# Kernel optimization log

Hardware: AMD Instinct MI355X
Metric: run time of the kernel (lower is better)

## Reference

```python
import jax, jax.numpy as jnp
import numpy as np

HEADS, HEAD_DIM = 8, 32
FOLD_W = FOLD_H = 8
PW = PH = 2  # proposal_w/h -> M = PW*PH centers per region


def setup_inputs() -> dict:
    key = jax.random.key(0)
    ks = jax.random.split(key, 8)
    dim, hd = 96, HEADS * HEAD_DIM
    return {
        "x": jax.random.normal(ks[0], (16, dim, 64, 64), jnp.float32),
        "Wf": jax.random.normal(ks[1], (hd, dim), jnp.float32) * 0.05,
        "bf": jax.random.normal(ks[2], (hd,), jnp.float32) * 0.01,
        "Wv": jax.random.normal(ks[3], (hd, dim), jnp.float32) * 0.05,
        "bv": jax.random.normal(ks[4], (hd,), jnp.float32) * 0.01,
        "Wp": jax.random.normal(ks[5], (dim, hd), jnp.float32) * 0.05,
        "bp": jax.random.normal(ks[6], (dim,), jnp.float32) * 0.01,
        "sim_alpha": jnp.ones((1,), jnp.float32),
        "sim_beta": jnp.zeros((1,), jnp.float32),
    }


def _l2norm(t):
    # matches torch F.normalize(dim=-1, eps=1e-12)
    n = jnp.maximum(jnp.linalg.norm(t, axis=-1, keepdims=True), 1e-12)
    return t / n


def _cluster_forward(x, Wf, bf, Wv, bv, Wp, bp, sim_alpha, sim_beta):
    B, C, W, H = x.shape
    # 1x1 convs
    v = jnp.einsum("bchw,oc->bohw", x, Wv) + bv[None, :, None, None]
    f = jnp.einsum("bchw,oc->bohw", x, Wf) + bf[None, :, None, None]

    def split_heads(t):  # b (e c) w h -> (b e) c w h
        b = t.shape[0]
        return t.reshape(b, HEADS, HEAD_DIM, W, H).reshape(b * HEADS, HEAD_DIM, W, H)

    f, v = split_heads(f), split_heads(v)

    def fold(t):  # b c (f1 w) (f2 h) -> (b f1 f2) c w h
        b, c, w0, h0 = t.shape
        ws, hs = w0 // FOLD_W, h0 // FOLD_H
        t = t.reshape(b, c, FOLD_W, ws, FOLD_H, hs)
        return t.transpose(0, 2, 4, 1, 3, 5).reshape(b * FOLD_W * FOLD_H, c, ws, hs)

    f, v = fold(f), fold(v)
    b, c, w, h = f.shape

    def pool(t):  # AdaptiveMaxPool2d((PW,PH)); divides evenly -> block max
        return t.reshape(b, c, PW, w // PW, PH, h // PH).max(axis=(3, 5))

    centers = pool(f).reshape(b, c, PW * PH).transpose(0, 2, 1)       # [b,M,c]
    value_centers = pool(v).reshape(b, c, PW * PH).transpose(0, 2, 1)  # [b,M,c]
    pts = f.reshape(b, c, w * h).transpose(0, 2, 1)                    # [b,N,c]

    cos = jnp.einsum("bmc,bnc->bmn", _l2norm(centers), _l2norm(pts))
    sim = jax.nn.sigmoid(sim_beta + sim_alpha * cos)                   # [b,M,N]

    # hard assignment: each point keeps only its best center
    idx = jnp.argmax(sim, axis=1)                                      # [b,N]
    mask = jax.nn.one_hot(idx, sim.shape[1], dtype=sim.dtype)          # [b,N,M]
    mask = jnp.transpose(mask, (0, 2, 1))                              # [b,M,N]
    sim = sim * mask

    value2 = v.reshape(b, c, w * h).transpose(0, 2, 1)                 # [b,N,c]
    # gather points -> centers
    agg = (jnp.einsum("bnc,bmn->bmc", value2, sim) + value_centers) / (
        mask.sum(axis=-1, keepdims=True) + 1.0
    )
    # dispatch centers -> points
    out = jnp.einsum("bmc,bmn->bnc", agg, sim)                         # [b,N,c]
    out = out.transpose(0, 2, 1).reshape(b, c, w, h)

    # unfold regions back
    bb = b // (FOLD_W * FOLD_H)
    out = out.reshape(bb, FOLD_W, FOLD_H, c, w, h).transpose(0, 3, 1, 4, 2, 5)
    out = out.reshape(bb, c, FOLD_W * w, FOLD_H * h)
    # merge heads: (b e) c w h -> b (e c) w h
    out = out.reshape(bb // HEADS, HEADS * HEAD_DIM, W, H)
    out = jnp.einsum("bchw,oc->bohw", out, Wp) + bp[None, :, None, None]
    return out


def reference(x, Wf, bf, Wv, bv, Wp, bp, sim_alpha, sim_beta):
    return _cluster_forward(x, Wf, bf, Wv, bv, Wp, bp, sim_alpha, sim_beta)
```

## Files before the change

### kernel.cpp

```cpp
#include <hip/hip_runtime.h>
#include <math.h>


#define TPB 256

__global__ __launch_bounds__(TPB, 4)
void cc_main(const float* __restrict__ x,
             const float* __restrict__ Wf, const float* __restrict__ bf,
             const float* __restrict__ Wv, const float* __restrict__ bv,
             const float* __restrict__ Wp,
             const float* __restrict__ salpha, const float* __restrict__ sbeta,
             float* __restrict__ cd)
{
    __shared__ __align__(16) float smem[8320];
    __shared__ float cfs[2][132], cvs[2][132], swb[2][256], aggs[2][132];
    __shared__ float2 bib[2][64];
    __shared__ float cnts[2][4];

    const int t    = threadIdx.x;
    const int lane = t & 63;
    const int wid  = __builtin_amdgcn_readfirstlane(t >> 6);
    const int tc   = t >> 4;
    const int tp   = t & 15;
    const int blk  = blockIdx.x;
    const int f1   = blk & 7;
    const int f2   = (blk >> 3) & 7;
    const int heg  = (blk >> 6) & 3;
    const int bb   = blk >> 8;
    const int fold = f1*8 + f2;

    const float* xb = x + (size_t)bb*96*4096 + (size_t)(f1*8)*64 + f2*8;

    float acc[8][4];
    {
        const float* bsrc = (tc < 8) ? (bf + heg*64 + tc*8)
                                     : (bv + heg*64 + (tc-8)*8);
        float4 b0 = *(const float4*)bsrc;
        float4 b1 = *(const float4*)(bsrc + 4);
        #pragma unroll
        for (int i = 0; i < 4; ++i) {
            acc[0][i]=b0.x; acc[1][i]=b0.y; acc[2][i]=b0.z; acc[3][i]=b0.w;
            acc[4][i]=b1.x; acc[5][i]=b1.y; acc[6][i]=b1.z; acc[7][i]=b1.w;
        }
    }

    int xoff[2], xdst[2];
    #pragma unroll
    for (int i = 0; i < 2; ++i) {
        int fl = i*256 + t;
        int kl = fl >> 4, sg = fl & 15;
        xoff[i] = kl*4096 + (sg >> 1)*64 + (sg & 1)*4;
        xdst[i] = 4096 + kl*64 + sg*4;
    }
    int wdst[4];
    const float* wptr[4];
    #pragma unroll
    for (int i = 0; i < 4; ++i) {
        int fl = i*256 + t;
        int rr = fl & 127, kq = fl >> 7;
        wptr[i] = ((rr < 64) ? (Wf + (size_t)(heg*64 + rr)*96)
                             : (Wv + (size_t)(heg*64 + rr - 64)*96)) + kq*4;
        wdst[i] = (kq*4)*128 + rr;
    }

    float4 pxr[2], pwr[4];
    #pragma unroll
    for (int i = 0; i < 2; ++i) pxr[i] = *(const float4*)(xb + xoff[i]);
    #pragma unroll
    for (int i = 0; i < 4; ++i) pwr[i] = *(const float4*)(wptr[i]);
    #pragma unroll
    for (int i = 0; i < 2; ++i) *(float4*)&smem[xdst[i]] = pxr[i];
    #pragma unroll
    for (int i = 0; i < 4; ++i) {
        smem[wdst[i]      ] = pwr[i].x;
        smem[wdst[i] + 128] = pwr[i].y;
        smem[wdst[i] + 256] = pwr[i].z;
        smem[wdst[i] + 384] = pwr[i].w;
    }
    __syncthreads();

    for (int kc = 0; ; ) {
        if (kc < 64) {
            #pragma unroll
            for (int i = 0; i < 2; ++i)
                pxr[i] = *(const float4*)(xb + (kc+32)*4096 + xoff[i]);
            #pragma unroll
            for (int i = 0; i < 4; ++i)
                pwr[i] = *(const float4*)(wptr[i] + kc + 32);
        }
        #pragma unroll 4
        for (int k = 0; k < 32; ++k) {
            float4 wa  = *(const float4*)&smem[k*128 + tc*8];
            float4 wb4 = *(const float4*)&smem[k*128 + tc*8 + 4];
            float4 xq  = *(const float4*)&smem[4096 + k*64 + tp*4];
            float xv[4] = {xq.x, xq.y, xq.z, xq.w};
            #pragma unroll
            for (int i = 0; i < 4; ++i) {
                acc[0][i] = fmaf(wa.x,  xv[i], acc[0][i]);
                acc[1][i] = fmaf(wa.y,  xv[i], acc[1][i]);
                acc[2][i] = fmaf(wa.z,  xv[i], acc[2][i]);
                acc[3][i] = fmaf(wa.w,  xv[i], acc[3][i]);
                acc[4][i] = fmaf(wb4.x, xv[i], acc[4][i]);
                acc[5][i] = fmaf(wb4.y, xv[i], acc[5][i]);
                acc[6][i] = fmaf(wb4.z, xv[i], acc[6][i]);
                acc[7][i] = fmaf(wb4.w, xv[i], acc[7][i]);
            }
        }
        if (kc == 64) break;
        __syncthreads();
        #pragma unroll
        for (int i = 0; i < 2; ++i) *(float4*)&smem[xdst[i]] = pxr[i];
        #pragma unroll
        for (int i = 0; i < 4; ++i) {
            smem[wdst[i]      ] = pwr[i].x;
            smem[wdst[i] + 128] = pwr[i].y;
            smem[wdst[i] + 256] = pwr[i].z;
            smem[wdst[i] + 384] = pwr[i].w;
        }
        __syncthreads();
        kc += 32;
    }

    const float alpha = salpha[0], beta = sbeta[0];
    __syncthreads();
    #pragma unroll
    for (int j = 0; j < 8; ++j)
        #pragma unroll
        for (int i2 = 0; i2 < 4; ++i2)
            smem[(tc*8 + j)*65 + tp*4 + i2] = acc[j][i2];
    __syncthreads();

    if (wid < 2) {
        const int he = wid, slot = he;
        {
            int m = lane >> 4, c0 = (lane & 15)*2;
            int pw = m >> 1, ph = m & 1;
            #pragma unroll
            for (int cc = 0; cc < 2; ++cc) {
                int c = c0 + cc;
                float mf = -3.402823466e38f, mv = -3.402823466e38f;
                #pragma unroll
                for (int a = 0; a < 4; ++a)
                    #pragma unroll
                    for (int b2 = 0; b2 < 4; ++b2) {
                        int n = (pw*4 + a)*8 + ph*4 + b2;
                        mf = fmaxf(mf, smem[(he*32 + c)*65 + n]);
                        mv = fmaxf(mv, smem[(64 + he*32 + c)*65 + n]);
                    }
                cfs[slot][m*33 + c] = mf;
                cvs[slot][m*33 + c] = mv;
            }
        }
        float d0=0,d1=0,d2=0,d3=0,pn=0,cn0=0,cn1=0,cn2=0,cn3=0;
        #pragma unroll 8
        for (int c = 0; c < 32; ++c) {
            float fv = smem[(he*32 + c)*65 + lane];
            float m0 = cfs[slot][c], m1 = cfs[slot][33+c];
            float m2 = cfs[slot][66+c], m3 = cfs[slot][99+c];
            d0 = fmaf(m0, fv, d0); d1 = fmaf(m1, fv, d1);
            d2 = fmaf(m2, fv, d2); d3 = fmaf(m3, fv, d3);
            pn = fmaf(fv, fv, pn);
            cn0 = fmaf(m0, m0, cn0); cn1 = fmaf(m1, m1, cn1);
            cn2 = fmaf(m2, m2, cn2); cn3 = fmaf(m3, m3, cn3);
        }
        float ip = 1.f / fmaxf(sqrtf(pn), 1e-12f);
        float z0 = beta + alpha*(d0*(1.f/fmaxf(sqrtf(cn0),1e-12f))*ip);
        float z1 = beta + alpha*(d1*(1.f/fmaxf(sqrtf(cn1),1e-12f))*ip);
        float z2 = beta + alpha*(d2*(1.f/fmaxf(sqrtf(cn2),1e-12f))*ip);
        float z3 = beta + alpha*(d3*(1.f/fmaxf(sqrtf(cn3),1e-12f))*ip);
        float s0 = 1.f/(1.f + expf(-z0));
        float s1 = 1.f/(1.f + expf(-z1));
        float s2 = 1.f/(1.f + expf(-z2));
        float s3 = 1.f/(1.f + expf(-z3));
        int bi = 0; float bvv = s0;
        if (s1 > bvv) { bvv = s1; bi = 1; }
        if (s2 > bvv) { bvv = s2; bi = 2; }
        if (s3 > bvv) { bvv = s3; bi = 3; }
        int cnt0 = __popcll(__ballot(bi == 0));
        int cnt1 = __popcll(__ballot(bi == 1));
        int cnt2 = __popcll(__ballot(bi == 2));
        int cnt3 = __popcll(__ballot(bi == 3));
        swb[slot][lane]       = (bi==0) ? bvv : 0.f;
        swb[slot][64 + lane]  = (bi==1) ? bvv : 0.f;
        swb[slot][128 + lane] = (bi==2) ? bvv : 0.f;
        swb[slot][192 + lane] = (bi==3) ? bvv : 0.f;
        bib[slot][lane] = make_float2(bvv, (float)bi);
        if (lane == 0) {
            cnts[slot][0] = (float)cnt0; cnts[slot][1] = (float)cnt1;
            cnts[slot][2] = (float)cnt2; cnts[slot][3] = (float)cnt3;
        }
    }
    __syncthreads();

    float* tb = cd + ((size_t)(bb*64 + fold))*4096;

    if (wid >= 2) {
        const int he = wid - 2, slot = he;
        const int cI = lane & 31;
        #pragma unroll
        for (int it = 0; it < 2; ++it) {
            int mm = it*2 + (lane >> 5);
            float s = 0.f;
            #pragma unroll 8
            for (int n2 = 0; n2 < 64; ++n2)
                s = fmaf(smem[(64 + he*32 + cI)*65 + n2],
                         swb[slot][mm*64 + n2], s);
            aggs[slot][mm*33 + cI] = (s + cvs[slot][mm*33 + cI])
                                   / (cnts[slot][mm] + 1.f);
        }
        float2 b2 = bib[slot][lane];
        *(float2*)&tb[3072 + (heg*2 + he)*128 + lane*2] = b2;
    }
    __syncthreads();

    #pragma unroll
    for (int it = 0; it < 3; ++it) {
        int idx = it*256 + t;
        int he  = (idx >= 384) ? 1 : 0;
        int rem = idx - he*384;
        int oc  = rem >> 2, m = rem & 3;
        const float* wp = Wp + (size_t)oc*256 + heg*64 + he*32;
        const float* ag = aggs[he] + m*33;
        float s = 0.f;
        #pragma unroll
        for (int c = 0; c < 32; ++c)
            s = fmaf(wp[c], ag[c], s);
        tb[(heg*2 + he)*384 + oc*4 + m] = s;
    }
}

__global__ __launch_bounds__(TPB, 8)
void cc_comb(const float* __restrict__ cd, const float* __restrict__ bp,
             float* __restrict__ out)
{
    __shared__ __align__(16) float ld[4096];
    const int t    = threadIdx.x;
    const int lane = t & 63;
    const int wid  = __builtin_amdgcn_readfirstlane(t >> 6);
    const int blk  = blockIdx.x;
    const int f1   = blk & 7;
    const int f2   = (blk >> 3) & 7;
    const int bb   = blk >> 6;
    const float* tb = cd + ((size_t)(bb*64 + f1*8 + f2))*4096;

    #pragma unroll
    for (int i = 0; i < 4; ++i) {
        float4 v = *(const float4*)(tb + (t*4 + i)*4);
        *(float4*)&ld[(t*4 + i)*4] = v;
    }
    __syncthreads();

    const int oc0 = wid*24;
    float acc[24];
    #pragma unroll
    for (int j = 0; j < 24; j += 4) {
        float4 b = *(const float4*)(bp + oc0 + j);
        acc[j]=b.x; acc[j+1]=b.y; acc[j+2]=b.z; acc[j+3]=b.w;
    }

    #pragma unroll
    for (int he = 0; he < 8; ++he) {
        float2 sv = *(const float2*)&ld[3072 + he*128 + lane*2];
        const int bi = (int)sv.y;
        const float s0 = (bi==0) ? sv.x : 0.f;
        const float s1 = (bi==1) ? sv.x : 0.f;
        const float s2 = (bi==2) ? sv.x : 0.f;
        const float s3 = (bi==3) ? sv.x : 0.f;
        const float* pr = &ld[he*384 + oc0*4];
        #pragma unroll
        for (int j = 0; j < 24; ++j) {
            float4 p = *(const float4*)(pr + j*4);
            acc[j] = fmaf(p.x, s0, acc[j]);
            acc[j] = fmaf(p.y, s1, acc[j]);
            acc[j] = fmaf(p.z, s2, acc[j]);
            acc[j] = fmaf(p.w, s3, acc[j]);
        }
    }

    const int r = lane >> 3, hh = lane & 7;
    const size_t ob = (size_t)bb*96*4096 + (size_t)(f1*8 + r)*64 + f2*8 + hh;
    #pragma unroll
    for (int j = 0; j < 24; ++j)
        out[ob + (size_t)(oc0 + j)*4096] = acc[j];
}

extern "C" void kernel_launch(void* const* d_in, const int* in_sizes, int n_in,
                              void* d_out, int out_size, void* d_ws, size_t ws_size,
                              hipStream_t stream) {
    (void)in_sizes; (void)n_in; (void)out_size; (void)ws_size;
    float* cd = (float*)d_ws;
    cc_main<<<dim3(4096), dim3(TPB), 0, stream>>>(
        (const float*)d_in[0],
        (const float*)d_in[1],
        (const float*)d_in[2],
        (const float*)d_in[3],
        (const float*)d_in[4],
        (const float*)d_in[5],
        (const float*)d_in[7],
        (const float*)d_in[8],
        cd);
    cc_comb<<<dim3(1024), dim3(TPB), 0, stream>>>(
        cd,
        (const float*)d_in[6],
        (float*)d_out);
}
```

Measured before the change: 211.5 us.

## Fuse combine stage into main kernel via atomic accumulation into bias-initialized output

Removes the separate combine kernel and workspace round-trip. A small init kernel fills the output with the projection bias, and each main block computes its two heads' contribution to every output channel and atomically adds it into the output. This avoids writing and re-reading the intermediate per-fold buffer. In exchange it issues four atomic adds per output element (one per head group), adds a barrier in the main kernel, and makes the float summation order nondeterministic.

```diff
diff --git a/kernel.cpp b/kernel.cpp
--- a/kernel.cpp
+++ b/kernel.cpp
@@ -3,6 +3,18 @@
 
 
 #define TPB 256
+
+__global__ __launch_bounds__(TPB, 8)
+void cc_init(const float* __restrict__ bp, float* __restrict__ out)
+{
+    const int oc = blockIdx.x % 96;
+    const float b = bp[oc];
+    const float4 v = make_float4(b, b, b, b);
+    float* o = out + (size_t)blockIdx.x * 4096 + threadIdx.x * 4;
+    #pragma unroll
+    for (int i = 0; i < 4; ++i)
+        *(float4*)(o + i*1024) = v;
+}
 
 __global__ __launch_bounds__(TPB, 4)
 void cc_main(const float* __restrict__ x,
@@ -10,7 +22,7 @@
              const float* __restrict__ Wv, const float* __restrict__ bv,
              const float* __restrict__ Wp,
              const float* __restrict__ salpha, const float* __restrict__ sbeta,
-             float* __restrict__ cd)
+             float* __restrict__ out)
 {
     __shared__ __align__(16) float smem[8320];
     __shared__ float cfs[2][132], cvs[2][132], swb[2][256], aggs[2][132];
@@ -27,7 +39,6 @@
     const int f2   = (blk >> 3) & 7;
     const int heg  = (blk >> 6) & 3;
     const int bb   = blk >> 8;
-    const int fold = f1*8 + f2;
 
     const float* xb = x + (size_t)bb*96*4096 + (size_t)(f1*8)*64 + f2*8;
 
@@ -192,8 +203,6 @@
     }
     __syncthreads();
 
-    float* tb = cd + ((size_t)(bb*64 + fold))*4096;
-
     if (wid >= 2) {
         const int he = wid - 2, slot = he;
         const int cI = lane & 31;
@@ -208,8 +217,6 @@
             aggs[slot][mm*33 + cI] = (s + cvs[slot][mm*33 + cI])
                                    / (cnts[slot][mm] + 1.f);
         }
-        float2 b2 = bib[slot][lane];
-        *(float2*)&tb[3072 + (heg*2 + he)*128 + lane*2] = b2;
     }
     __syncthreads();
 
@@ -225,70 +232,49 @@
         #pragma unroll
         for (int c = 0; c < 32; ++c)
             s = fmaf(wp[c], ag[c], s);
-        tb[(heg*2 + he)*384 + oc*4 + m] = s;
-    }
-}
-
-__global__ __launch_bounds__(TPB, 8)
-void cc_comb(const float* __restrict__ cd, const float* __restrict__ bp,
-             float* __restrict__ out)
-{
-    __shared__ __align__(16) float ld[4096];
-    const int t    = threadIdx.x;
-    const int lane = t & 63;
-    const int wid  = __builtin_amdgcn_readfirstlane(t >> 6);
-    const int blk  = blockIdx.x;
-    const int f1   = blk & 7;
-    const int f2   = (blk >> 3) & 7;
-    const int bb   = blk >> 6;
-    const float* tb = cd + ((size_t)(bb*64 + f1*8 + f2))*4096;
-
-    #pragma unroll
-    for (int i = 0; i < 4; ++i) {
-        float4 v = *(const float4*)(tb + (t*4 + i)*4);
-        *(float4*)&ld[(t*4 + i)*4] = v;
-    }
-    __syncthreads();
-
-    const int oc0 = wid*24;
-    float acc[24];
-    #pragma unroll
-    for (int j = 0; j < 24; j += 4) {
-        float4 b = *(const float4*)(bp + oc0 + j);
-        acc[j]=b.x; acc[j+1]=b.y; acc[j+2]=b.z; acc[j+3]=b.w;
-    }
-
-    #pragma unroll
-    for (int he = 0; he < 8; ++he) {
-        float2 sv = *(const float2*)&ld[3072 + he*128 + lane*2];
-        const int bi = (int)sv.y;
-        const float s0 = (bi==0) ? sv.x : 0.f;
-        const float s1 = (bi==1) ? sv.x : 0.f;
-        const float s2 = (bi==2) ? sv.x : 0.f;
-        const float s3 = (bi==3) ? sv.x : 0.f;
-        const float* pr = &ld[he*384 + oc0*4];
-        #pragma unroll
-        for (int j = 0; j < 24; ++j) {
-            float4 p = *(const float4*)(pr + j*4);
-            acc[j] = fmaf(p.x, s0, acc[j]);
-            acc[j] = fmaf(p.y, s1, acc[j]);
-            acc[j] = fmaf(p.z, s2, acc[j]);
-            acc[j] = fmaf(p.w, s3, acc[j]);
-        }
-    }
-
-    const int r = lane >> 3, hh = lane & 7;
-    const size_t ob = (size_t)bb*96*4096 + (size_t)(f1*8 + r)*64 + f2*8 + hh;
-    #pragma unroll
-    for (int j = 0; j < 24; ++j)
-        out[ob + (size_t)(oc0 + j)*4096] = acc[j];
+        smem[he*384 + oc*4 + m] = s;
+    }
+    __syncthreads();
+
+    {
+        const int oc0 = wid*24;
+        float con[24];
+        #pragma unroll
+        for (int j = 0; j < 24; ++j) con[j] = 0.f;
+        #pragma unroll
+        for (int he = 0; he < 2; ++he) {
+            float2 sv = bib[he][lane];
+            const int bi = (int)sv.y;
+            const float s0 = (bi==0) ? sv.x : 0.f;
+            const float s1 = (bi==1) ? sv.x : 0.f;
+            const float s2 = (bi==2) ? sv.x : 0.f;
+            const float s3 = (bi==3) ? sv.x : 0.f;
+            const float* pr = &smem[he*384 + oc0*4];
+            #pragma unroll
+            for (int j = 0; j < 24; ++j) {
+                float4 p = *(const float4*)(pr + j*4);
+                con[j] = fmaf(p.x, s0, con[j]);
+                con[j] = fmaf(p.y, s1, con[j]);
+                con[j] = fmaf(p.z, s2, con[j]);
+                con[j] = fmaf(p.w, s3, con[j]);
+            }
+        }
+        const int r = lane >> 3, hh = lane & 7;
+        const size_t ob = (size_t)bb*96*4096
+                        + (size_t)(f1*8 + r)*64 + f2*8 + hh;
+        #pragma unroll
+        for (int j = 0; j < 24; ++j)
+            atomicAdd(&out[ob + (size_t)(oc0 + j)*4096], con[j]);
+    }
 }
 
 extern "C" void kernel_launch(void* const* d_in, const int* in_sizes, int n_in,
                               void* d_out, int out_size, void* d_ws, size_t ws_size,
                               hipStream_t stream) {
-    (void)in_sizes; (void)n_in; (void)out_size; (void)ws_size;
-    float* cd = (float*)d_ws;
+    (void)in_sizes; (void)n_in; (void)out_size; (void)d_ws; (void)ws_size;
+    cc_init<<<dim3(1536), dim3(TPB), 0, stream>>>(
+        (const float*)d_in[6],
+        (float*)d_out);
     cc_main<<<dim3(4096), dim3(TPB), 0, stream>>>(
         (const float*)d_in[0],
         (const float*)d_in[1],
@@ -298,9 +284,5 @@
         (const float*)d_in[5],
         (const float*)d_in[7],
         (const float*)d_in[8],
-        cd);
-    cc_comb<<<dim3(1024), dim3(TPB), 0, stream>>>(
-        cd,
-        (const float*)d_in[6],
         (float*)d_out);
 }
```

New measurement: 264.7 us. 1.25x slower.

## Process two fold regions per block with 8x8 register tiles in projection GEMM

Applied to the files above, without the earlier changes.

Each block now covers two adjacent fold regions (128 pixels) instead of one, so the 1x1-conv GEMM uses an 8x8 per-thread register tile, doubling arithmetic per shared-memory load and halving weight reloads per pixel. The K chunk shrinks from 32 to 16 to keep shared memory within budget. The clustering epilogue then runs twice in a loop, once per fold. The grid is halved, and the larger accumulator tile raises register pressure, which may reduce occupancy under launch_bounds(256,4).

```diff
diff --git a/kernel.cpp b/kernel.cpp
--- a/kernel.cpp
+++ b/kernel.cpp
@@ -20,42 +20,38 @@
     const int t    = threadIdx.x;
     const int lane = t & 63;
     const int wid  = __builtin_amdgcn_readfirstlane(t >> 6);
-    const int tc   = t >> 4;
-    const int tp   = t & 15;
+    const int cg   = t >> 4;
+    const int pg   = t & 15;
     const int blk  = blockIdx.x;
     const int f1   = blk & 7;
-    const int f2   = (blk >> 3) & 7;
-    const int heg  = (blk >> 6) & 3;
-    const int bb   = blk >> 8;
-    const int fold = f1*8 + f2;
-
-    const float* xb = x + (size_t)bb*96*4096 + (size_t)(f1*8)*64 + f2*8;
-
-    float acc[8][4];
+    const int f2p  = (blk >> 3) & 3;
+    const int heg  = (blk >> 5) & 3;
+    const int bb   = blk >> 7;
+
+    const float* xb = x + (size_t)bb*96*4096 + (size_t)(f1*8)*64 + f2p*16;
+
+    float acc[8][8];
     {
-        const float* bsrc = (tc < 8) ? (bf + heg*64 + tc*8)
-                                     : (bv + heg*64 + (tc-8)*8);
-        float4 b0 = *(const float4*)bsrc;
-        float4 b1 = *(const float4*)(bsrc + 4);
-        #pragma unroll
-        for (int i = 0; i < 4; ++i) {
-            acc[0][i]=b0.x; acc[1][i]=b0.y; acc[2][i]=b0.z; acc[3][i]=b0.w;
-            acc[4][i]=b1.x; acc[5][i]=b1.y; acc[6][i]=b1.z; acc[7][i]=b1.w;
-        }
+        const float* bsrc = ((cg < 8) ? bf : bv) + heg*64 + (cg & 7)*8;
+        float4 b0 = *(const float4*)bsrc, b1 = *(const float4*)(bsrc + 4);
+        float bj[8] = {b0.x,b0.y,b0.z,b0.w,b1.x,b1.y,b1.z,b1.w};
+        #pragma unroll
+        for (int j = 0; j < 8; ++j)
+            #pragma unroll
+            for (int i = 0; i < 8; ++i) acc[j][i] = bj[j];
     }
 
     int xoff[2], xdst[2];
     #pragma unroll
     for (int i = 0; i < 2; ++i) {
         int fl = i*256 + t;
-        int kl = fl >> 4, sg = fl & 15;
-        xoff[i] = kl*4096 + (sg >> 1)*64 + (sg & 1)*4;
-        xdst[i] = 4096 + kl*64 + sg*4;
-    }
-    int wdst[4];
-    const float* wptr[4];
-    #pragma unroll
-    for (int i = 0; i < 4; ++i) {
+        int kl = fl >> 5, p4 = (fl & 31)*4;
+        xoff[i] = kl*4096 + ((p4 & 63) >> 3)*64 + (p4 >> 6)*8 + (p4 & 7);
+        xdst[i] = 2048 + kl*128 + p4;
+    }
+    int wdst[2]; const float* wptr[2];
+    #pragma unroll
+    for (int i = 0; i < 2; ++i) {
         int fl = i*256 + t;
         int rr = fl & 127, kq = fl >> 7;
         wptr[i] = ((rr < 64) ? (Wf + (size_t)(heg*64 + rr)*96)
@@ -63,15 +59,15 @@
         wdst[i] = (kq*4)*128 + rr;
     }
 
-    float4 pxr[2], pwr[4];
+    float4 pxr[2], pwr[2];
     #pragma unroll
     for (int i = 0; i < 2; ++i) pxr[i] = *(const float4*)(xb + xoff[i]);
     #pragma unroll
-    for (int i = 0; i < 4; ++i) pwr[i] = *(const float4*)(wptr[i]);
+    for (int i = 0; i < 2; ++i) pwr[i] = *(const float4*)(wptr[i]);
     #pragma unroll
     for (int i = 0; i < 2; ++i) *(float4*)&smem[xdst[i]] = pxr[i];
     #pragma unroll
-    for (int i = 0; i < 4; ++i) {
+    for (int i = 0; i < 2; ++i) {
         smem[wdst[i]      ] = pwr[i].x;
         smem[wdst[i] + 128] = pwr[i].y;
         smem[wdst[i] + 256] = pwr[i].z;
@@ -80,152 +76,155 @@
     __syncthreads();
 
     for (int kc = 0; ; ) {
-        if (kc < 64) {
+        if (kc < 80) {
             #pragma unroll
             for (int i = 0; i < 2; ++i)
-                pxr[i] = *(const float4*)(xb + (kc+32)*4096 + xoff[i]);
-            #pragma unroll
-            for (int i = 0; i < 4; ++i)
-                pwr[i] = *(const float4*)(wptr[i] + kc + 32);
+                pxr[i] = *(const float4*)(xb + (kc+16)*4096 + xoff[i]);
+            #pragma unroll
+            for (int i = 0; i < 2; ++i)
+                pwr[i] = *(const float4*)(wptr[i] + kc + 16);
         }
         #pragma unroll 4
-        for (int k = 0; k < 32; ++k) {
-            float4 wa  = *(const float4*)&smem[k*128 + tc*8];
-            float4 wb4 = *(const float4*)&smem[k*128 + tc*8 + 4];
-            float4 xq  = *(const float4*)&smem[4096 + k*64 + tp*4];
-            float xv[4] = {xq.x, xq.y, xq.z, xq.w};
-            #pragma unroll
-            for (int i = 0; i < 4; ++i) {
-                acc[0][i] = fmaf(wa.x,  xv[i], acc[0][i]);
-                acc[1][i] = fmaf(wa.y,  xv[i], acc[1][i]);
-                acc[2][i] = fmaf(wa.z,  xv[i], acc[2][i]);
-                acc[3][i] = fmaf(wa.w,  xv[i], acc[3][i]);
-                acc[4][i] = fmaf(wb4.x, xv[i], acc[4][i]);
-                acc[5][i] = fmaf(wb4.y, xv[i], acc[5][i]);
-                acc[6][i] = fmaf(wb4.z, xv[i], acc[6][i]);
-                acc[7][i] = fmaf(wb4.w, xv[i], acc[7][i]);
-            }
-        }
-        if (kc == 64) break;
+        for (int k = 0; k < 16; ++k) {
+            float4 wa = *(const float4*)&smem[k*128 + cg*8];
+            float4 wb = *(const float4*)&smem[k*128 + cg*8 + 4];
+            float4 xa = *(const float4*)&smem[2048 + k*128 + pg*8];
+            float4 xc = *(const float4*)&smem[2048 + k*128 + pg*8 + 4];
+            float wv[8] = {wa.x,wa.y,wa.z,wa.w,wb.x,wb.y,wb.z,wb.w};
+            float xv[8] = {xa.x,xa.y,xa.z,xa.w,xc.x,xc.y,xc.z,xc.w};
+            #pragma unroll
+            for (int j = 0; j < 8; ++j)
+                #pragma unroll
+                for (int i = 0; i < 8; ++i)
+                    acc[j][i] = fmaf(wv[j], xv[i], acc[j][i]);
+        }
+        if (kc == 80) break;
         __syncthreads();
         #pragma unroll
         for (int i = 0; i < 2; ++i) *(float4*)&smem[xdst[i]] = pxr[i];
         #pragma unroll
-        for (int i = 0; i < 4; ++i) {
+        for (int i = 0; i < 2; ++i) {
             smem[wdst[i]      ] = pwr[i].x;
             smem[wdst[i] + 128] = pwr[i].y;
             smem[wdst[i] + 256] = pwr[i].z;
             smem[wdst[i] + 384] = pwr[i].w;
         }
         __syncthreads();
-        kc += 32;
+        kc += 16;
     }
 
     const float alpha = salpha[0], beta = sbeta[0];
-    __syncthreads();
-    #pragma unroll
-    for (int j = 0; j < 8; ++j)
-        #pragma unroll
-        for (int i2 = 0; i2 < 4; ++i2)
-            smem[(tc*8 + j)*65 + tp*4 + i2] = acc[j][i2];
-    __syncthreads();
-
-    if (wid < 2) {
-        const int he = wid, slot = he;
-        {
-            int m = lane >> 4, c0 = (lane & 15)*2;
-            int pw = m >> 1, ph = m & 1;
-            #pragma unroll
-            for (int cc = 0; cc < 2; ++cc) {
-                int c = c0 + cc;
-                float mf = -3.402823466e38f, mv = -3.402823466e38f;
+
+    for (int fl = 0; fl < 2; ++fl) {
+        __syncthreads();
+        if ((pg >> 3) == fl) {
+            const int nb = (pg & 7)*8;
+            #pragma unroll
+            for (int j = 0; j < 8; ++j)
                 #pragma unroll
-                for (int a = 0; a < 4; ++a)
+                for (int i = 0; i < 8; ++i)
+                    smem[(cg*8 + j)*65 + nb + i] = acc[j][i];
+        }
+        __syncthreads();
+
+        if (wid < 2) {
+            const int he = wid, slot = he;
+            {
+                int m = lane >> 4, c0 = (lane & 15)*2;
+                int pw = m >> 1, ph = m & 1;
+                #pragma unroll
+                for (int cc = 0; cc < 2; ++cc) {
+                    int c = c0 + cc;
+                    float mf = -3.402823466e38f, mv = -3.402823466e38f;
                     #pragma unroll
-                    for (int b2 = 0; b2 < 4; ++b2) {
-                        int n = (pw*4 + a)*8 + ph*4 + b2;
-                        mf = fmaxf(mf, smem[(he*32 + c)*65 + n]);
-                        mv = fmaxf(mv, smem[(64 + he*32 + c)*65 + n]);
-                    }
-                cfs[slot][m*33 + c] = mf;
-                cvs[slot][m*33 + c] = mv;
+                    for (int a = 0; a < 4; ++a)
+                        #pragma unroll
+                        for (int b2 = 0; b2 < 4; ++b2) {
+                            int n = (pw*4 + a)*8 + ph*4 + b2;
+                            mf = fmaxf(mf, smem[(he*32 + c)*65 + n]);
+                            mv = fmaxf(mv, smem[(64 + he*32 + c)*65 + n]);
+                        }
+                    cfs[slot][m*33 + c] = mf;
+                    cvs[slot][m*33 + c] = mv;
+                }
             }
-        }
-        float d0=0,d1=0,d2=0,d3=0,pn=0,cn0=0,cn1=0,cn2=0,cn3=0;
-        #pragma unroll 8
-        for (int c = 0; c < 32; ++c) {
-            float fv = smem[(he*32 + c)*65 + lane];
-            float m0 = cfs[slot][c], m1 = cfs[slot][33+c];
-            float m2 = cfs[slot][66+c], m3 = cfs[slot][99+c];
-            d0 = fmaf(m0, fv, d0); d1 = fmaf(m1, fv, d1);
-            d2 = fmaf(m2, fv, d2); d3 = fmaf(m3, fv, d3);
-            pn = fmaf(fv, fv, pn);
-            cn0 = fmaf(m0, m0, cn0); cn1 = fmaf(m1, m1, cn1);
-            cn2 = fmaf(m2, m2, cn2); cn3 = fmaf(m3, m3, cn3);
-        }
-        float ip = 1.f / fmaxf(sqrtf(pn), 1e-12f);
-        float z0 = beta + alpha*(d0*(1.f/fmaxf(sqrtf(cn0),1e-12f))*ip);
-        float z1 = beta + alpha*(d1*(1.f/fmaxf(sqrtf(cn1),1e-12f))*ip);
-        float z2 = beta + alpha*(d2*(1.f/fmaxf(sqrtf(cn2),1e-12f))*ip);
-        float z3 = beta + alpha*(d3*(1.f/fmaxf(sqrtf(cn3),1e-12f))*ip);
-        float s0 = 1.f/(1.f + expf(-z0));
-        float s1 = 1.f/(1.f + expf(-z1));
-        float s2 = 1.f/(1.f + expf(-z2));
-        float s3 = 1.f/(1.f + expf(-z3));
-        int bi = 0; float bvv = s0;
-        if (s1 > bvv) { bvv = s1; bi = 1; }
-        if (s2 > bvv) { bvv = s2; bi = 2; }
-        if (s3 > bvv) { bvv = s3; bi = 3; }
-        int cnt0 = __popcll(__ballot(bi == 0));
-        int cnt1 = __popcll(__ballot(bi == 1));
-        int cnt2 = __popcll(__ballot(bi == 2));
-        int cnt3 = __popcll(__ballot(bi == 3));
-        swb[slot][lane]       = (bi==0) ? bvv : 0.f;
-        swb[slot][64 + lane]  = (bi==1) ? bvv : 0.f;
-        swb[slot][128 + lane] = (bi==2) ? bvv : 0.f;
-        swb[slot][192 + lane] = (bi==3) ? bvv : 0.f;
-        bib[slot][lane] = make_float2(bvv, (float)bi);
-        if (lane == 0) {
-            cnts[slot][0] = (float)cnt0; cnts[slot][1] = (float)cnt1;
-            cnts[slot][2] = (float)cnt2; cnts[slot][3] = (float)cnt3;
-        }
-    }
-    __syncthreads();
-
-    float* tb = cd + ((size_t)(bb*64 + fold))*4096;
-
-    if (wid >= 2) {
-        const int he = wid - 2, slot = he;
-        const int cI = lane & 31;
-        #pragma unroll
-        for (int it = 0; it < 2; ++it) {
-            int mm = it*2 + (lane >> 5);
+            float d0=0,d1=0,d2=0,d3=0,pn=0,cn0=0,cn1=0,cn2=0,cn3=0;
+            #pragma unroll 8
+            for (int c = 0; c < 32; ++c) {
+                float fv = smem[(he*32 + c)*65 + lane];
+                float m0 = cfs[slot][c], m1 = cfs[slot][33+c];
+                float m2 = cfs[slot][66+c], m3 = cfs[slot][99+c];
+                d0 = fmaf(m0, fv, d0); d1 = fmaf(m1, fv, d1);
+                d2 = fmaf(m2, fv, d2); d3 = fmaf(m3, fv, d3);
+                pn = fmaf(fv, fv, pn);
+                cn0 = fmaf(m0, m0, cn0); cn1 = fmaf(m1, m1, cn1);
+                cn2 = fmaf(m2, m2, cn2); cn3 = fmaf(m3, m3, cn3);
+            }
+            float ip = 1.f / fmaxf(sqrtf(pn), 1e-12f);
+            float z0 = beta + alpha*(d0*(1.f/fmaxf(sqrtf(cn0),1e-12f))*ip);
+            float z1 = beta + alpha*(d1*(1.f/fmaxf(sqrtf(cn1),1e-12f))*ip);
+            float z2 = beta + alpha*(d2*(1.f/fmaxf(sqrtf(cn2),1e-12f))*ip);
+            float z3 = beta + alpha*(d3*(1.f/fmaxf(sqrtf(cn3),1e-12f))*ip);
+            float s0 = 1.f/(1.f + expf(-z0));
+            float s1 = 1.f/(1.f + expf(-z1));
+            float s2 = 1.f/(1.f + expf(-z2));
+            float s3 = 1.f/(1.f + expf(-z3));
+            int bi = 0; float bvv = s0;
+            if (s1 > bvv) { bvv = s1; bi = 1; }
+            if (s2 > bvv) { bvv = s2; bi = 2; }
+            if (s3 > bvv) { bvv = s3; bi = 3; }
+            int cnt0 = __popcll(__ballot(bi == 0));
+            int cnt1 = __popcll(__ballot(bi == 1));
+            int cnt2 = __popcll(__ballot(bi == 2));
+            int cnt3 = __popcll(__ballot(bi == 3));
+            swb[slot][lane]       = (bi==0) ? bvv : 0.f;
+            swb[slot][64 + lane]  = (bi==1) ? bvv : 0.f;
+            swb[slot][128 + lane] = (bi==2) ? bvv : 0.f;
+            swb[slot][192 + lane] = (bi==3) ? bvv : 0.f;
+            bib[slot][lane] = make_float2(bvv, (float)bi);
+            if (lane == 0) {
+                cnts[slot][0] = (float)cnt0; cnts[slot][1] = (float)cnt1;
+                cnts[slot][2] = (float)cnt2; cnts[slot][3] = (float)cnt3;
+            }
+        }
+        __syncthreads();
+
+        const int fold = f1*8 + f2p*2 + fl;
+        float* tb = cd + ((size_t)(bb*64 + fold))*4096;
+
+        if (wid >= 2) {
+            const int he = wid - 2, slot = he;
+            const int cI = lane & 31;
+            #pragma unroll
+            for (int it = 0; it < 2; ++it) {
+                int mm = it*2 + (lane >> 5);
+                float s = 0.f;
+                #pragma unroll 8
+                for (int n2 = 0; n2 < 64; ++n2)
+                    s = fmaf(smem[(64 + he*32 + cI)*65 + n2],
+                             swb[slot][mm*64 + n2], s);
+                aggs[slot][mm*33 + cI] = (s + cvs[slot][mm*33 + cI])
+                                       / (cnts[slot][mm] + 1.f);
+            }
+            float2 b2 = bib[slot][lane];
+            *(float2*)&tb[3072 + (heg*2 + he)*128 + lane*2] = b2;
+        }
+        __syncthreads();
+
+        #pragma unroll
+        for (int it = 0; it < 3; ++it) {
+            int idx = it*256 + t;
+            int he  = (idx >= 384) ? 1 : 0;
+            int rem = idx - he*384;
+            int oc  = rem >> 2, m = rem & 3;
+            const float* wp = Wp + (size_t)oc*256 + heg*64 + he*32;
+            const float* ag = aggs[he] + m*33;
             float s = 0.f;
-            #pragma unroll 8
-            for (int n2 = 0; n2 < 64; ++n2)
-                s = fmaf(smem[(64 + he*32 + cI)*65 + n2],
-                         swb[slot][mm*64 + n2], s);
-            aggs[slot][mm*33 + cI] = (s + cvs[slot][mm*33 + cI])
-                                   / (cnts[slot][mm] + 1.f);
-        }
-        float2 b2 = bib[slot][lane];
-        *(float2*)&tb[3072 + (heg*2 + he)*128 + lane*2] = b2;
-    }
-    __syncthreads();
-
-    #pragma unroll
-    for (int it = 0; it < 3; ++it) {
-        int idx = it*256 + t;
-        int he  = (idx >= 384) ? 1 : 0;
-        int rem = idx - he*384;
-        int oc  = rem >> 2, m = rem & 3;
-        const float* wp = Wp + (size_t)oc*256 + heg*64 + he*32;
-        const float* ag = aggs[he] + m*33;
-        float s = 0.f;
-        #pragma unroll
-        for (int c = 0; c < 32; ++c)
-            s = fmaf(wp[c], ag[c], s);
-        tb[(heg*2 + he)*384 + oc*4 + m] = s;
+            #pragma unroll
+            for (int c = 0; c < 32; ++c)
+                s = fmaf(wp[c], ag[c], s);
+            tb[(heg*2 + he)*384 + oc*4 + m] = s;
+        }
     }
 }
 
@@ -289,7 +288,7 @@
                               hipStream_t stream) {
     (void)in_sizes; (void)n_in; (void)out_size; (void)ws_size;
     float* cd = (float*)d_ws;
-    cc_main<<<dim3(4096), dim3(TPB), 0, stream>>>(
+    cc_main<<<dim3(2048), dim3(TPB), 0, stream>>>(
         (const float*)d_in[0],
         (const float*)d_in[1],
         (const float*)d_in[2],
```

After: 213.2 us. Within noise of the previous version (+0.8%).

## Keep value projection in registers, compute pooling and aggregation via shuffles

Applied to the files above, without the earlier changes.

Only the f-projection accumulators are stored to shared memory now; the v-projection stays in registers. Value-center max pooling and the point-to-center aggregation are done directly from registers with cross-lane shuffle reductions. This shrinks the shared buffer so launch bounds can request 5 blocks per SM, cutting LDS traffic and raising occupancy. The cost is extra shuffle work and more register pressure from the 32-element accumulator array, which may be hard to fit under the tighter bound.

```diff
diff --git a/kernel.cpp b/kernel.cpp
--- a/kernel.cpp
+++ b/kernel.cpp
@@ -4,7 +4,7 @@
 
 #define TPB 256
 
-__global__ __launch_bounds__(TPB, 4)
+__global__ __launch_bounds__(TPB, 5)
 void cc_main(const float* __restrict__ x,
              const float* __restrict__ Wf, const float* __restrict__ bf,
              const float* __restrict__ Wv, const float* __restrict__ bv,
@@ -12,7 +12,7 @@
              const float* __restrict__ salpha, const float* __restrict__ sbeta,
              float* __restrict__ cd)
 {
-    __shared__ __align__(16) float smem[8320];
+    __shared__ __align__(16) float smem[6144];
     __shared__ float cfs[2][132], cvs[2][132], swb[2][256], aggs[2][132];
     __shared__ float2 bib[2][64];
     __shared__ float cnts[2][4];
@@ -123,11 +123,26 @@
 
     const float alpha = salpha[0], beta = sbeta[0];
     __syncthreads();
-    #pragma unroll
-    for (int j = 0; j < 8; ++j)
-        #pragma unroll
-        for (int i2 = 0; i2 < 4; ++i2)
-            smem[(tc*8 + j)*65 + tp*4 + i2] = acc[j][i2];
+
+    if (wid < 2) {
+        #pragma unroll
+        for (int j = 0; j < 8; ++j)
+            #pragma unroll
+            for (int i2 = 0; i2 < 4; ++i2)
+                smem[(tc*8 + j)*65 + tp*4 + i2] = acc[j][i2];
+    } else {
+        const int he = wid - 2;
+        const int m  = ((tp >> 3) << 1) | (tp & 1);
+        const int c0 = ((tc - 8) & 3) * 8;
+        #pragma unroll
+        for (int j = 0; j < 8; ++j) {
+            float mv = fmaxf(fmaxf(acc[j][0], acc[j][1]),
+                             fmaxf(acc[j][2], acc[j][3]));
+            mv = fmaxf(mv, __shfl_xor(mv, 2));
+            mv = fmaxf(mv, __shfl_xor(mv, 4));
+            if ((tp & 6) == 0) cvs[he][m*33 + c0 + j] = mv;
+        }
+    }
     __syncthreads();
 
     if (wid < 2) {
@@ -138,17 +153,15 @@
             #pragma unroll
             for (int cc = 0; cc < 2; ++cc) {
                 int c = c0 + cc;
-                float mf = -3.402823466e38f, mv = -3.402823466e38f;
+                float mf = -3.402823466e38f;
                 #pragma unroll
                 for (int a = 0; a < 4; ++a)
                     #pragma unroll
                     for (int b2 = 0; b2 < 4; ++b2) {
                         int n = (pw*4 + a)*8 + ph*4 + b2;
                         mf = fmaxf(mf, smem[(he*32 + c)*65 + n]);
-                        mv = fmaxf(mv, smem[(64 + he*32 + c)*65 + n]);
                     }
                 cfs[slot][m*33 + c] = mf;
-                cvs[slot][m*33 + c] = mv;
             }
         }
         float d0=0,d1=0,d2=0,d3=0,pn=0,cn0=0,cn1=0,cn2=0,cn3=0;
@@ -196,17 +209,48 @@
 
     if (wid >= 2) {
         const int he = wid - 2, slot = he;
-        const int cI = lane & 31;
-        #pragma unroll
-        for (int it = 0; it < 2; ++it) {
-            int mm = it*2 + (lane >> 5);
-            float s = 0.f;
-            #pragma unroll 8
-            for (int n2 = 0; n2 < 64; ++n2)
-                s = fmaf(smem[(64 + he*32 + cI)*65 + n2],
-                         swb[slot][mm*64 + n2], s);
-            aggs[slot][mm*33 + cI] = (s + cvs[slot][mm*33 + cI])
-                                   / (cnts[slot][mm] + 1.f);
+        const int c0 = ((tc - 8) & 3) * 8;
+        float s[8][4];
+        #pragma unroll
+        for (int j = 0; j < 8; ++j)
+            #pragma unroll
+            for (int m = 0; m < 4; ++m) s[j][m] = 0.f;
+        #pragma unroll
+        for (int i = 0; i < 4; ++i) {
+            int n = tp*4 + i;
+            float w0 = swb[slot][n],       w1 = swb[slot][64 + n];
+            float w2 = swb[slot][128 + n], w3 = swb[slot][192 + n];
+            #pragma unroll
+            for (int j = 0; j < 8; ++j) {
+                float v = acc[j][i];
+                s[j][0] = fmaf(v, w0, s[j][0]);
+                s[j][1] = fmaf(v, w1, s[j][1]);
+                s[j][2] = fmaf(v, w2, s[j][2]);
+                s[j][3] = fmaf(v, w3, s[j][3]);
+            }
+        }
+        #pragma unroll
+        for (int j = 0; j < 8; ++j)
+            #pragma unroll
+            for (int m = 0; m < 4; ++m) {
+                float v = s[j][m];
+                v += __shfl_xor(v, 1);
+                v += __shfl_xor(v, 2);
+                v += __shfl_xor(v, 4);
+                v += __shfl_xor(v, 8);
+                s[j][m] = v;
+            }
+        if (tp == 0) {
+            #pragma unroll
+            for (int m = 0; m < 4; ++m) {
+                float inv = 1.f;
+                #pragma unroll
+                for (int j = 0; j < 8; ++j)
+                    aggs[slot][m*33 + c0 + j] =
+                        (s[j][m] + cvs[slot][m*33 + c0 + j])
+                        / (cnts[slot][m] + 1.f);
+                (void)inv;
+            }
         }
         float2 b2 = bib[slot][lane];
         *(float2*)&tb[3072 + (heg*2 + he)*128 + lane*2] = b2;
```

Measured after the change: 214.5 us. Within noise of the previous version (+1.4%).
